# Kernel tuning notes

Measured on AMD Instinct MI355X. Metric: run time of the kernel, lower is better.

The kernel has to match this reference:

```python
import jax, jax.numpy as jnp
import numpy as np

B = 32          # decode batch (num sequences)
H = 32          # query heads
HKV = 8         # kv heads (GQA group = H // HKV = 4)
DH = 128        # head dim
MAX_LIVE = 2048 # compact cache budget per sequence (max_live_count)
S = B * MAX_LIVE  # total compact slots
SCALE = DH ** -0.5


def setup_inputs() -> dict:
    key = jax.random.key(0)
    ks = jax.random.split(key, 6)
    q = jax.random.normal(ks[0], (B, H, DH), dtype=jnp.float32)
    k = jax.random.normal(ks[1], (B, HKV, DH), dtype=jnp.float32)
    v = jax.random.normal(ks[2], (B, HKV, DH), dtype=jnp.float32)
    compact_k_cache = jax.random.normal(ks[3], (S, HKV, DH), dtype=jnp.float32)
    compact_v_cache = jax.random.normal(ks[4], (S, HKV, DH), dtype=jnp.float32)
    base_offsets = (jnp.arange(B, dtype=jnp.int32) * MAX_LIVE)
    live_counts = jax.random.randint(ks[5], (B,), 1, MAX_LIVE + 1).astype(jnp.int32)
    # new token is stored at the last live slot of each sequence
    slot_mapping = base_offsets + live_counts - 1
    return {
        "q": q, "k": k, "v": v,
        "compact_k_cache": compact_k_cache,
        "compact_v_cache": compact_v_cache,
        "base_offsets": base_offsets,
        "live_counts": live_counts,
        "slot_mapping": slot_mapping,
    }


def reference(q, k, v, compact_k_cache, compact_v_cache,
              base_offsets, live_counts, slot_mapping):
    # ---- store_compact_kvcache: scatter new token k/v into compact caches ----
    valid = slot_mapping >= 0                       # slot == -1 -> skip
    safe_slot = jnp.where(valid, slot_mapping, 0)
    m = valid[:, None, None]
    kc = compact_k_cache.at[safe_slot].set(
        jnp.where(m, k, compact_k_cache[safe_slot]))
    vc = compact_v_cache.at[safe_slot].set(
        jnp.where(m, v, compact_v_cache[safe_slot]))

    # ---- compact_decode_attention over [base_offset, base_offset+live_count) ----
    pos = jnp.arange(MAX_LIVE, dtype=jnp.int32)            # [L]
    mask = pos[None, :] < live_counts[:, None]             # [B, L]
    idx = base_offsets[:, None] + pos[None, :]             # [B, L]
    safe_idx = jnp.where(mask, idx, 0)
    kg = kc[safe_idx]                                      # [B, L, HKV, DH]
    vg = vc[safe_idx]                                      # [B, L, HKV, DH]

    G = H // HKV
    qg = q.reshape(B, HKV, G, DH)                          # group query heads by kv head
    scores = jnp.einsum('bhgd,blhd->bhgl', qg, kg) * SCALE # [B, HKV, G, L]
    scores = jnp.where(mask[:, None, None, :], scores, jnp.finfo(scores.dtype).min)
    p = jax.nn.softmax(scores, axis=-1)
    o = jnp.einsum('bhgl,blhd->bhgd', p, vg).reshape(B, H, DH)
    return o
```

## Files before the change

### kernel.cpp

```cpp
#include <hip/hip_runtime.h>
#include <math.h>

#define NB 32
#define NH 32
#define NKV 8
#define NG 4
#define DH 128
#define MAXL 2048
#define CHUNK 256
#define NCH (MAXL / CHUNK)

#define SCALE_LOG2E 0.12752966529379885f

__global__ __launch_bounds__(256) void attn_partial_kernel(
    const float* __restrict__ q,
    const float* __restrict__ knew,
    const float* __restrict__ vnew,
    const float* __restrict__ kcache,
    const float* __restrict__ vcache,
    const int* __restrict__ base_offsets,
    const int* __restrict__ live_counts,
    const int* __restrict__ slot_mapping,
    float* __restrict__ pml,
    float* __restrict__ pacc)
{
    const int c = blockIdx.x;
    const int h = blockIdx.y;
    const int b = blockIdx.z;

    const int live = live_counts[b];
    const int p0 = c * CHUNK;
    if (p0 >= live) return;

    const int base = base_offsets[b];
    const int slot = slot_mapping[b];

    const int tid  = (int)threadIdx.x;
    const int wave = tid >> 6;
    const int lane = tid & 63;
    const int half = lane >> 5;
    const int ql   = lane & 31;

    float4 qv[NG];
#pragma unroll
    for (int g = 0; g < NG; ++g)
        qv[g] = *(const float4*)(q + (size_t)(b * NH + h * NG + g) * DH + ql * 4);

    float m[NG], l[NG];
    float4 acc[NG];
#pragma unroll
    for (int g = 0; g < NG; ++g) {
        m[g] = -INFINITY;
        l[g] = 0.f;
        acc[g] = make_float4(0.f, 0.f, 0.f, 0.f);
    }

    const size_t rowstride = (size_t)NKV * DH;
    const float* kbase = kcache + ((size_t)base * NKV + h) * DH + ql * 4;
    const float* vbase = vcache + ((size_t)base * NKV + h) * DH + ql * 4;

    const int pw0 = p0 + wave * 64;
    const int rem = live - pw0;
    const int iters = (rem <= 0) ? 0 : (rem >= 64 ? 32 : ((rem + 1) >> 1));

    int p = pw0 + half;
    float4 kv = make_float4(0.f, 0.f, 0.f, 0.f), vv = kv;
    if (p < live) {
        kv = *(const float4*)(kbase + (size_t)p * rowstride);
        vv = *(const float4*)(vbase + (size_t)p * rowstride);
    }

    for (int i = 0; i < iters; ++i) {
        const int pn = p + 2;
        float4 kn = make_float4(0.f, 0.f, 0.f, 0.f), vn = kn;
        if (i + 1 < iters && pn < live) {
            kn = *(const float4*)(kbase + (size_t)pn * rowstride);
            vn = *(const float4*)(vbase + (size_t)pn * rowstride);
        }

        if (p < live) {
            float4 kk = kv, vx = vv;
            if (base + p == slot) {
                kk = *(const float4*)(knew + (size_t)(b * NKV + h) * DH + ql * 4);
                vx = *(const float4*)(vnew + (size_t)(b * NKV + h) * DH + ql * 4);
            }
#pragma unroll
            for (int g = 0; g < NG; ++g) {
                float d = kk.x * qv[g].x + kk.y * qv[g].y +
                          kk.z * qv[g].z + kk.w * qv[g].w;
                d += __shfl_xor(d, 1);
                d += __shfl_xor(d, 2);
                d += __shfl_xor(d, 4);
                d += __shfl_xor(d, 8);
                d += __shfl_xor(d, 16);
                const float s     = d * SCALE_LOG2E;
                const float mn    = fmaxf(m[g], s);
                const float alpha = exp2f(m[g] - mn);
                const float pw    = exp2f(s - mn);
                l[g] = l[g] * alpha + pw;
                acc[g].x = acc[g].x * alpha + pw * vx.x;
                acc[g].y = acc[g].y * alpha + pw * vx.y;
                acc[g].z = acc[g].z * alpha + pw * vx.z;
                acc[g].w = acc[g].w * alpha + pw * vx.w;
                m[g] = mn;
            }
        }
        kv = kn; vv = vn; p = pn;
    }

    __shared__ float sm[NG][8], sl[NG][8];
    __shared__ float4 sacc[NG][8][32];
    const int hw = wave * 2 + half;
#pragma unroll
    for (int g = 0; g < NG; ++g) {
        if (ql == 0) { sm[g][hw] = m[g]; sl[g][hw] = l[g]; }
        sacc[g][hw][ql] = acc[g];
    }
    __syncthreads();

    const int g = wave;
    float M = -INFINITY;
#pragma unroll
    for (int j = 0; j < 8; ++j) M = fmaxf(M, sm[g][j]);
    float L = 0.f, w8[8];
#pragma unroll
    for (int j = 0; j < 8; ++j) {
        w8[j] = exp2f(sm[g][j] - M);
        L += w8[j] * sl[g][j];
    }

    if (half == 0) {
        float4 o = make_float4(0.f, 0.f, 0.f, 0.f);
#pragma unroll
        for (int j = 0; j < 8; ++j) {
            const float4 a = sacc[g][j][ql];
            o.x += w8[j] * a.x; o.y += w8[j] * a.y;
            o.z += w8[j] * a.z; o.w += w8[j] * a.w;
        }
        const size_t pidx = ((size_t)(b * NKV + h) * NG + g) * NCH + c;
        if (ql == 0) { pml[pidx * 2] = M; pml[pidx * 2 + 1] = L; }
        *(float4*)(pacc + pidx * DH + ql * 4) = o;
    }
}

__global__ __launch_bounds__(256) void attn_combine_kernel(
    const int* __restrict__ live_counts,
    const float* __restrict__ pml,
    const float* __restrict__ pacc,
    float* __restrict__ out)
{
    const int h = blockIdx.x;
    const int b = blockIdx.y;
    const int g = (int)threadIdx.x >> 6;
    const int lane = (int)threadIdx.x & 63;

    const int live = live_counts[b];
    const int nc = (live + CHUNK - 1) / CHUNK;
    const size_t pbase = ((size_t)(b * NKV + h) * NG + g) * NCH;

    float M = -INFINITY;
    float mv[NCH], lv[NCH];
    for (int cj = 0; cj < nc; ++cj) {
        mv[cj] = pml[(pbase + cj) * 2];
        lv[cj] = pml[(pbase + cj) * 2 + 1];
        M = fmaxf(M, mv[cj]);
    }
    float L = 0.f, w[NCH];
    for (int cj = 0; cj < nc; ++cj) {
        w[cj] = exp2f(mv[cj] - M);
        L += w[cj] * lv[cj];
    }
    const float inv = 1.f / L;

    float2 o = make_float2(0.f, 0.f);
    for (int cj = 0; cj < nc; ++cj) {
        const float2 a = *(const float2*)(pacc + (pbase + cj) * DH + lane * 2);
        o.x += w[cj] * a.x;
        o.y += w[cj] * a.y;
    }
    o.x *= inv; o.y *= inv;
    *(float2*)(out + (size_t)(b * NH + h * NG + g) * DH + lane * 2) = o;
}

extern "C" void kernel_launch(void* const* d_in, const int* in_sizes, int n_in,
                              void* d_out, int out_size, void* d_ws, size_t ws_size,
                              hipStream_t stream) {
    const float* q    = (const float*)d_in[0];
    const float* knew = (const float*)d_in[1];
    const float* vnew = (const float*)d_in[2];
    const float* kc   = (const float*)d_in[3];
    const float* vc   = (const float*)d_in[4];
    const int* base   = (const int*)d_in[5];
    const int* live   = (const int*)d_in[6];
    const int* slot   = (const int*)d_in[7];
    float* out = (float*)d_out;

    float* pml  = (float*)d_ws;
    float* pacc = pml + (size_t)2 * NB * NKV * NG * NCH;

    dim3 grid1(NCH, NKV, NB);
    attn_partial_kernel<<<grid1, 256, 0, stream>>>(q, knew, vnew, kc, vc,
                                                   base, live, slot, pml, pacc);
    dim3 grid2(NKV, NB);
    attn_combine_kernel<<<grid2, 256, 0, stream>>>(live, pml, pacc, out);
}
```

Measured before the change: 514.9 us.

## Restructure partial attention into two-pass score/softmax with unrolled loads and DPP reductions

Replaces the per-token online-softmax loop with a two-phase scheme. All K rows in a chunk are first loaded in a fully unrolled loop with clamped addresses, and scores are written to shared memory. A block-wide softmax follows, then a second unrolled pass accumulates V with the precomputed weights. The chunk size is halved to give more blocks, and the cross-lane dot-product reduction uses DPP instead of shuffles. The aim is to expose far more outstanding memory loads and remove the per-token exp/rescale work, in exchange for extra shared memory, more partials, and wasted loads on clamped tail rows.

```diff
diff --git a/kernel.cpp b/kernel.cpp
--- a/kernel.cpp
+++ b/kernel.cpp
@@ -7,10 +7,25 @@
 #define NG 4
 #define DH 128
 #define MAXL 2048
-#define CHUNK 256
+#define CHUNK 128
 #define NCH (MAXL / CHUNK)
+#define ROWF (NKV * DH)
 
 #define SCALE_LOG2E 0.12752966529379885f
+
+template <int CTRL>
+__device__ __forceinline__ float dpp_add(float x) {
+    int y = __builtin_amdgcn_update_dpp(0, __float_as_int(x), CTRL, 0xf, 0xf, false);
+    return x + __int_as_float(y);
+}
+__device__ __forceinline__ float half_reduce_sum(float d) {
+    d = dpp_add<0x111>(d);
+    d = dpp_add<0x112>(d);
+    d = dpp_add<0x114>(d);
+    d = dpp_add<0x118>(d);
+    d = dpp_add<0x142>(d);
+    return d;
+}
 
 __global__ __launch_bounds__(256) void attn_partial_kernel(
     const float* __restrict__ q,
@@ -33,7 +48,7 @@
     if (p0 >= live) return;
 
     const int base = base_offsets[b];
-    const int slot = slot_mapping[b];
+    const int rep  = slot_mapping[b] - base;
 
     const int tid  = (int)threadIdx.x;
     const int wave = tid >> 6;
@@ -41,104 +56,99 @@
     const int half = lane >> 5;
     const int ql   = lane & 31;
 
+    __shared__ float  sc[NG][CHUNK];
+    __shared__ float4 sacc[NG][8][32];
+
     float4 qv[NG];
 #pragma unroll
     for (int g = 0; g < NG; ++g)
         qv[g] = *(const float4*)(q + (size_t)(b * NH + h * NG + g) * DH + ql * 4);
 
-    float m[NG], l[NG];
+    const float4 kn4 = *(const float4*)(knew + (size_t)(b * NKV + h) * DH + ql * 4);
+    const float4 vn4 = *(const float4*)(vnew + (size_t)(b * NKV + h) * DH + ql * 4);
+
+    const int lim = live - 1;
+    const int pw0 = p0 + wave * 32;
+    const float* kb = kcache + (size_t)base * ROWF + h * DH + ql * 4;
+    const float* vb = vcache + (size_t)base * ROWF + h * DH + ql * 4;
+
+#pragma unroll
+    for (int i = 0; i < 16; ++i) {
+        const int p  = pw0 + 2 * i + half;
+        const int pc = min(p, lim);
+        float4 kk = *(const float4*)(kb + ((size_t)pc << 10));
+        if (pc == rep) kk = kn4;
+#pragma unroll
+        for (int g = 0; g < NG; ++g) {
+            float d = kk.x * qv[g].x + kk.y * qv[g].y +
+                      kk.z * qv[g].z + kk.w * qv[g].w;
+            d = half_reduce_sum(d);
+            const float s = (p <= lim) ? d * SCALE_LOG2E : -INFINITY;
+            if (ql == 31) sc[g][p - p0] = s;
+        }
+    }
+    __syncthreads();
+
+    {
+        const int g = wave;
+        const float s0 = sc[g][lane];
+        const float s1 = sc[g][64 + lane];
+        float m = fmaxf(s0, s1);
+#pragma unroll
+        for (int off = 1; off < 64; off <<= 1)
+            m = fmaxf(m, __shfl_xor(m, off));
+        const float e0 = exp2f(s0 - m);
+        const float e1 = exp2f(s1 - m);
+        float l = e0 + e1;
+#pragma unroll
+        for (int off = 1; off < 64; off <<= 1)
+            l += __shfl_xor(l, off);
+        sc[g][lane]      = e0;
+        sc[g][64 + lane] = e1;
+        if (lane == 0) {
+            const size_t pidx = ((size_t)(b * NKV + h) * NG + g) * NCH + c;
+            pml[pidx * 2]     = m;
+            pml[pidx * 2 + 1] = l;
+        }
+    }
+    __syncthreads();
+
     float4 acc[NG];
 #pragma unroll
-    for (int g = 0; g < NG; ++g) {
-        m[g] = -INFINITY;
-        l[g] = 0.f;
-        acc[g] = make_float4(0.f, 0.f, 0.f, 0.f);
-    }
-
-    const size_t rowstride = (size_t)NKV * DH;
-    const float* kbase = kcache + ((size_t)base * NKV + h) * DH + ql * 4;
-    const float* vbase = vcache + ((size_t)base * NKV + h) * DH + ql * 4;
-
-    const int pw0 = p0 + wave * 64;
-    const int rem = live - pw0;
-    const int iters = (rem <= 0) ? 0 : (rem >= 64 ? 32 : ((rem + 1) >> 1));
-
-    int p = pw0 + half;
-    float4 kv = make_float4(0.f, 0.f, 0.f, 0.f), vv = kv;
-    if (p < live) {
-        kv = *(const float4*)(kbase + (size_t)p * rowstride);
-        vv = *(const float4*)(vbase + (size_t)p * rowstride);
-    }
-
-    for (int i = 0; i < iters; ++i) {
-        const int pn = p + 2;
-        float4 kn = make_float4(0.f, 0.f, 0.f, 0.f), vn = kn;
-        if (i + 1 < iters && pn < live) {
-            kn = *(const float4*)(kbase + (size_t)pn * rowstride);
-            vn = *(const float4*)(vbase + (size_t)pn * rowstride);
-        }
-
-        if (p < live) {
-            float4 kk = kv, vx = vv;
-            if (base + p == slot) {
-                kk = *(const float4*)(knew + (size_t)(b * NKV + h) * DH + ql * 4);
-                vx = *(const float4*)(vnew + (size_t)(b * NKV + h) * DH + ql * 4);
-            }
-#pragma unroll
-            for (int g = 0; g < NG; ++g) {
-                float d = kk.x * qv[g].x + kk.y * qv[g].y +
-                          kk.z * qv[g].z + kk.w * qv[g].w;
-                d += __shfl_xor(d, 1);
-                d += __shfl_xor(d, 2);
-                d += __shfl_xor(d, 4);
-                d += __shfl_xor(d, 8);
-                d += __shfl_xor(d, 16);
-                const float s     = d * SCALE_LOG2E;
-                const float mn    = fmaxf(m[g], s);
-                const float alpha = exp2f(m[g] - mn);
-                const float pw    = exp2f(s - mn);
-                l[g] = l[g] * alpha + pw;
-                acc[g].x = acc[g].x * alpha + pw * vx.x;
-                acc[g].y = acc[g].y * alpha + pw * vx.y;
-                acc[g].z = acc[g].z * alpha + pw * vx.z;
-                acc[g].w = acc[g].w * alpha + pw * vx.w;
-                m[g] = mn;
-            }
-        }
-        kv = kn; vv = vn; p = pn;
-    }
-
-    __shared__ float sm[NG][8], sl[NG][8];
-    __shared__ float4 sacc[NG][8][32];
+    for (int g = 0; g < NG; ++g) acc[g] = make_float4(0.f, 0.f, 0.f, 0.f);
+
+#pragma unroll
+    for (int i = 0; i < 16; ++i) {
+        const int p  = pw0 + 2 * i + half;
+        const int pc = min(p, lim);
+        float4 vv = *(const float4*)(vb + ((size_t)pc << 10));
+        if (pc == rep) vv = vn4;
+        const int pos = p - p0;
+#pragma unroll
+        for (int g = 0; g < NG; ++g) {
+            const float w = sc[g][pos];
+            acc[g].x += w * vv.x;
+            acc[g].y += w * vv.y;
+            acc[g].z += w * vv.z;
+            acc[g].w += w * vv.w;
+        }
+    }
+
     const int hw = wave * 2 + half;
 #pragma unroll
-    for (int g = 0; g < NG; ++g) {
-        if (ql == 0) { sm[g][hw] = m[g]; sl[g][hw] = l[g]; }
+    for (int g = 0; g < NG; ++g)
         sacc[g][hw][ql] = acc[g];
-    }
     __syncthreads();
 
-    const int g = wave;
-    float M = -INFINITY;
-#pragma unroll
-    for (int j = 0; j < 8; ++j) M = fmaxf(M, sm[g][j]);
-    float L = 0.f, w8[8];
-#pragma unroll
-    for (int j = 0; j < 8; ++j) {
-        w8[j] = exp2f(sm[g][j] - M);
-        L += w8[j] * sl[g][j];
-    }
-
     if (half == 0) {
+        const int g = wave;
         float4 o = make_float4(0.f, 0.f, 0.f, 0.f);
 #pragma unroll
         for (int j = 0; j < 8; ++j) {
             const float4 a = sacc[g][j][ql];
-            o.x += w8[j] * a.x; o.y += w8[j] * a.y;
-            o.z += w8[j] * a.z; o.w += w8[j] * a.w;
+            o.x += a.x; o.y += a.y; o.z += a.z; o.w += a.w;
         }
         const size_t pidx = ((size_t)(b * NKV + h) * NG + g) * NCH + c;
-        if (ql == 0) { pml[pidx * 2] = M; pml[pidx * 2 + 1] = L; }
         *(float4*)(pacc + pidx * DH + ql * 4) = o;
     }
 }
@@ -159,25 +169,19 @@
     const size_t pbase = ((size_t)(b * NKV + h) * NG + g) * NCH;
 
     float M = -INFINITY;
-    float mv[NCH], lv[NCH];
-    for (int cj = 0; cj < nc; ++cj) {
-        mv[cj] = pml[(pbase + cj) * 2];
-        lv[cj] = pml[(pbase + cj) * 2 + 1];
-        M = fmaxf(M, mv[cj]);
-    }
-    float L = 0.f, w[NCH];
-    for (int cj = 0; cj < nc; ++cj) {
-        w[cj] = exp2f(mv[cj] - M);
-        L += w[cj] * lv[cj];
-    }
-    const float inv = 1.f / L;
-
+    for (int cj = 0; cj < nc; ++cj)
+        M = fmaxf(M, pml[(pbase + cj) * 2]);
+    float L = 0.f;
+    for (int cj = 0; cj < nc; ++cj)
+        L += exp2f(pml[(pbase + cj) * 2] - M) * pml[(pbase + cj) * 2 + 1];
     float2 o = make_float2(0.f, 0.f);
     for (int cj = 0; cj < nc; ++cj) {
+        const float w = exp2f(pml[(pbase + cj) * 2] - M);
         const float2 a = *(const float2*)(pacc + (pbase + cj) * DH + lane * 2);
-        o.x += w[cj] * a.x;
-        o.y += w[cj] * a.y;
-    }
+        o.x += w * a.x;
+        o.y += w * a.y;
+    }
+    const float inv = 1.f / L;
     o.x *= inv; o.y *= inv;
     *(float2*)(out + (size_t)(b * NH + h * NG + g) * DH + lane * 2) = o;
 }
```

New measurement: 487.4 us. -5.3%, faster.
